# Optimization experiments

Hardware: AMD Instinct MI355X
Metric: run time of the kernel (lower is better)

Reference implementation:

```python
import jax, jax.numpy as jnp
import numpy as np

QMAX = 127.0
QMIN = -128.0


def setup_inputs() -> dict:
    key = jax.random.key(0)
    k1, k2, k3 = jax.random.split(key, 3)
    B, N, D, O = 4, 4096, 2048, 2048
    x = jax.random.normal(k1, (B, N, D), dtype=jnp.float32)
    weight = jax.random.normal(k2, (O, D), dtype=jnp.float32)
    bias = jax.random.normal(k3, (O,), dtype=jnp.float32)
    return {"x": x, "weight": weight, "bias": bias}


def reference(x, weight, bias):
    # --- per-row symmetric int8 quantization of the weight [O, D] ---
    w_max = jnp.clip(jnp.max(jnp.abs(weight), axis=1, keepdims=True), 1e-8, None)
    w_scale = (w_max / QMAX)                     # [O, 1]
    w_q = jnp.clip(jnp.round(weight / w_scale), QMIN, QMAX).astype(jnp.int8)
    w_scale = w_scale.squeeze(1).astype(jnp.float32)  # [O]

    # --- dynamic per-row symmetric int8 quantization of x [B, N, D] ---
    x_max = jnp.max(jnp.abs(x), axis=2, keepdims=True)       # [B, N, 1]
    x_scale = jnp.maximum(x_max / QMAX, 1e-12)               # [B, N, 1]
    x_q = jnp.clip(jnp.round(x / x_scale), QMIN, QMAX).astype(jnp.int8)

    # --- int8 GEMM accumulated in int32: [B,N,D] x [O,D]^T -> [B,N,O] ---
    acc = jnp.einsum("bnd,od->bno", x_q.astype(jnp.int32), w_q.astype(jnp.int32))

    # --- dequantize with per-row activation scale and per-out-channel weight scale ---
    y = acc.astype(jnp.float32) * x_scale.astype(jnp.float32) * w_scale[None, None, :]
    y = y + bias
    return y.astype(x.dtype)
```

## Files before the change

kernel.cpp:

```cpp
#include <hip/hip_runtime.h>
#include <stdint.h>
#include <stddef.h>

typedef int v4i __attribute__((ext_vector_type(4)));

#define GLOAD_LDS16(g, l) __builtin_amdgcn_global_load_lds( \
    (const __attribute__((address_space(1))) void*)(g),     \
    (__attribute__((address_space(3))) void*)(l), 16, 0, 0)

__device__ __forceinline__ int pack4(float4 f, float s) {
    int a = (int)rintf(f.x / s); a = a < -128 ? -128 : (a > 127 ? 127 : a);
    int b = (int)rintf(f.y / s); b = b < -128 ? -128 : (b > 127 ? 127 : b);
    int c = (int)rintf(f.z / s); c = c < -128 ? -128 : (c > 127 ? 127 : c);
    int d = (int)rintf(f.w / s); d = d < -128 ? -128 : (d > 127 ? 127 : d);
    return (a & 255) | ((b & 255) << 8) | ((c & 255) << 16) | ((d & 255) << 24);
}

__global__ __launch_bounds__(256) void quant_rows_2048(
    const float* __restrict__ in, signed char* __restrict__ q,
    float* __restrict__ scales, float floorv)
{
    const int lane = threadIdx.x & 63;
    const int row  = blockIdx.x * 4 + (threadIdx.x >> 6);
    const float* rp = in + (size_t)row * 2048;

    float4 v[8];
#pragma unroll
    for (int j = 0; j < 2; ++j) {
        const float4* p = (const float4*)(rp + j * 1024 + lane * 16);
#pragma unroll
        for (int i = 0; i < 4; ++i) v[j * 4 + i] = p[i];
    }
    float am = 0.0f;
#pragma unroll
    for (int i = 0; i < 8; ++i) {
        am = fmaxf(am, fabsf(v[i].x));
        am = fmaxf(am, fabsf(v[i].y));
        am = fmaxf(am, fabsf(v[i].z));
        am = fmaxf(am, fabsf(v[i].w));
    }
#pragma unroll
    for (int off = 32; off; off >>= 1) am = fmaxf(am, __shfl_xor(am, off));
    const float s = fmaxf(am / 127.0f, floorv);

#pragma unroll
    for (int j = 0; j < 2; ++j) {
        int4 pk;
        pk.x = pack4(v[j * 4 + 0], s);
        pk.y = pack4(v[j * 4 + 1], s);
        pk.z = pack4(v[j * 4 + 2], s);
        pk.w = pack4(v[j * 4 + 3], s);
        *(int4*)(q + (size_t)row * 2048 + j * 1024 + lane * 16) = pk;
    }
    if (lane == 0) scales[row] = s;
}

__global__ __launch_bounds__(512, 4) void gemm_i8_ring(
    const signed char* __restrict__ xq, const signed char* __restrict__ wq,
    const float* __restrict__ xs, const float* __restrict__ ws,
    const float* __restrict__ bias, float* __restrict__ out, int K)
{
    __shared__ __align__(16) signed char lds[73728];

    const int tid  = threadIdx.x;
    const int lane = tid & 63;
    const int wid  = tid >> 6;
    const int wm   = wid >> 2;
    const int wn   = wid & 3;

    const int nwg  = gridDim.x * gridDim.y;
    int orig = blockIdx.y * gridDim.x + blockIdx.x;
    int swz  = ((nwg & 7) == 0) ? ((orig & 7) * (nwg >> 3) + (orig >> 3)) : orig;
    const int brow = (swz / gridDim.x) * 128;
    const int bcol = (swz % gridDim.x) * 256;

    const int gch  = (((tid & 3) ^ ((tid >> 3) & 3)) << 4);
    const int lofs = tid << 4;
    const signed char* gA  = xq + (size_t)(brow + (tid >> 2)) * K;
    const signed char* gB0 = wq + (size_t)(bcol + (tid >> 2)) * K;
    const signed char* gB1 = wq + (size_t)(bcol + 128 + (tid >> 2)) * K;

#define BUFOFF(bb) ((bb) * 24576)
#define ST3(tt, bb) do {                                                         \
    GLOAD_LDS16(gA  + (size_t)(tt) * 64 + gch, lds + BUFOFF(bb) + lofs);         \
    GLOAD_LDS16(gB0 + (size_t)(tt) * 64 + gch, lds + BUFOFF(bb) + 8192 + lofs);  \
    GLOAD_LDS16(gB1 + (size_t)(tt) * 64 + gch, lds + BUFOFF(bb) + 16384 + lofs); \
} while (0)

    const int rl   = lane & 15;
    const int ko   = lane >> 4;
    const int slot = ((ko ^ ((rl >> 1) & 3)) << 4);

#define FRAG_A(bb, r) (*(const v4i*)(lds + BUFOFF(bb) + (r) * 64 + slot))
#define FRAG_B(bb, r) (*(const v4i*)(lds + BUFOFF(bb) + 8192 + (r) * 64 + slot))

    v4i acc[4][4] = {};
    const int ar = wm * 64 + rl;
    const int br = wn * 64 + rl;

    ST3(0, 0);
    ST3(1, 1);
    asm volatile("s_waitcnt vmcnt(3)" ::: "memory");
    __builtin_amdgcn_s_barrier();

    const int NT = K >> 6;
    for (int t = 0; t < NT; ++t) {
        const int buf = t % 3;

        v4i af[4], bf[4];
#pragma unroll
        for (int m = 0; m < 4; ++m) af[m] = FRAG_A(buf, ar + m * 16);
#pragma unroll
        for (int n = 0; n < 4; ++n) bf[n] = FRAG_B(buf, br + n * 16);

        if (t + 2 < NT) ST3(t + 2, (t + 2) % 3);

#pragma unroll
        for (int m = 0; m < 4; ++m)
#pragma unroll
            for (int n = 0; n < 4; ++n)
                acc[m][n] = __builtin_amdgcn_mfma_i32_16x16x64_i8(
                    af[m], bf[n], acc[m][n], 0, 0, 0);

        if (t + 2 < NT) {
            asm volatile("s_waitcnt vmcnt(3) lgkmcnt(0)" ::: "memory");
            __builtin_amdgcn_s_barrier();
        } else if (t + 2 == NT) {
            asm volatile("s_waitcnt vmcnt(0) lgkmcnt(0)" ::: "memory");
            __builtin_amdgcn_s_barrier();
        }
    }

    const int rg = lane >> 4;
#pragma unroll
    for (int n = 0; n < 4; ++n) {
        const int col = bcol + wn * 64 + n * 16 + rl;
        const float wsc = ws[col];
        const float bv  = bias[col];
#pragma unroll
        for (int m = 0; m < 4; ++m) {
#pragma unroll
            for (int j = 0; j < 4; ++j) {
                const int row = brow + wm * 64 + m * 16 + rg * 4 + j;
                out[(size_t)row * 2048 + col] =
                    (float)acc[m][n][j] * xs[row] * wsc + bv;
            }
        }
    }
#undef ST3
#undef BUFOFF
#undef FRAG_A
#undef FRAG_B
}

extern "C" void kernel_launch(void* const* d_in, const int* in_sizes, int n_in,
                              void* d_out, int out_size, void* d_ws, size_t ws_size,
                              hipStream_t stream) {
    const float* x    = (const float*)d_in[0];
    const float* w    = (const float*)d_in[1];
    const float* bias = (const float*)d_in[2];
    float* out = (float*)d_out;

    const int D = 2048;
    const int O = in_sizes[2];
    const int M = in_sizes[0] / D;

    char* wsb = (char*)d_ws;
    signed char* xq  = (signed char*)wsb;
    signed char* wqp = (signed char*)(wsb + (size_t)M * D);
    float* xs  = (float*)(wsb + (size_t)M * D + (size_t)O * D);
    float* wsc = (float*)(wsb + (size_t)M * D + (size_t)O * D + (size_t)M * 4);

    quant_rows_2048<<<M / 4, 256, 0, stream>>>(x, xq, xs, 1e-12f);
    quant_rows_2048<<<O / 4, 256, 0, stream>>>(w, wqp, wsc, 1e-8f / 127.0f);

    dim3 grid(O / 256, M / 128);
    gemm_i8_ring<<<grid, 512, 0, stream>>>(xq, wqp, xs, wsc, bias, out, D);
}
```

Before: 126.3 us.

## Shrink GEMM tile to 128x128 with 4 waves and fuse quant launches

The GEMM workgroup tile drops from 128x256 with 8 waves to 128x128 with 4 waves. Each wave still computes a 64x64 sub-tile, and the three-stage LDS ring shrinks to 48KB. The intent is to fit more workgroups per CU and spread the work over a grid twice as large, at the cost of less reuse of the A tile per block. The two quantization launches are also merged into a single kernel that picks x or w by block index, saving one launch.

```diff
diff --git a/kernel.cpp b/kernel.cpp
--- a/kernel.cpp
+++ b/kernel.cpp
@@ -16,12 +16,20 @@
     return (a & 255) | ((b & 255) << 8) | ((c & 255) << 16) | ((d & 255) << 24);
 }
 
-__global__ __launch_bounds__(256) void quant_rows_2048(
-    const float* __restrict__ in, signed char* __restrict__ q,
-    float* __restrict__ scales, float floorv)
+__global__ __launch_bounds__(256) void quant_both_2048(
+    const float* __restrict__ x, signed char* __restrict__ xq,
+    float* __restrict__ xs,
+    const float* __restrict__ w, signed char* __restrict__ wq,
+    float* __restrict__ wsc, int nx4)
 {
     const int lane = threadIdx.x & 63;
-    const int row  = blockIdx.x * 4 + (threadIdx.x >> 6);
+    const bool isx = ((int)blockIdx.x < nx4);
+    const int rb   = isx ? blockIdx.x : (blockIdx.x - nx4);
+    const int row  = rb * 4 + (threadIdx.x >> 6);
+    const float* in = isx ? x : w;
+    signed char* q  = isx ? xq : wq;
+    float* scales   = isx ? xs : wsc;
+    const float floorv = isx ? 1e-12f : (1e-8f / 127.0f);
     const float* rp = in + (size_t)row * 2048;
 
     float4 v[8];
@@ -55,52 +63,50 @@
     if (lane == 0) scales[row] = s;
 }
 
-__global__ __launch_bounds__(512, 4) void gemm_i8_ring(
+__global__ __launch_bounds__(256, 3) void gemm_i8_r3s(
     const signed char* __restrict__ xq, const signed char* __restrict__ wq,
     const float* __restrict__ xs, const float* __restrict__ ws,
     const float* __restrict__ bias, float* __restrict__ out, int K)
 {
-    __shared__ __align__(16) signed char lds[73728];
+    __shared__ __align__(16) signed char lds[49152];
 
     const int tid  = threadIdx.x;
     const int lane = tid & 63;
     const int wid  = tid >> 6;
-    const int wm   = wid >> 2;
-    const int wn   = wid & 3;
+    const int wm   = wid >> 1;
+    const int wn   = wid & 1;
 
     const int nwg  = gridDim.x * gridDim.y;
     int orig = blockIdx.y * gridDim.x + blockIdx.x;
     int swz  = ((nwg & 7) == 0) ? ((orig & 7) * (nwg >> 3) + (orig >> 3)) : orig;
     const int brow = (swz / gridDim.x) * 128;
-    const int bcol = (swz % gridDim.x) * 256;
+    const int bcol = (swz % gridDim.x) * 128;
 
-    const int gch  = (((tid & 3) ^ ((tid >> 3) & 3)) << 4);
-    const int lofs = tid << 4;
-    const signed char* gA  = xq + (size_t)(brow + (tid >> 2)) * K;
-    const signed char* gB0 = wq + (size_t)(bcol + (tid >> 2)) * K;
-    const signed char* gB1 = wq + (size_t)(bcol + 128 + (tid >> 2)) * K;
+    const int gch = (((tid & 3) ^ ((tid >> 3) & 3)) << 4);
+    const signed char* gA = xq + (size_t)(brow + (tid >> 2)) * K;
+    const signed char* gB = wq + (size_t)(bcol + (tid >> 2)) * K;
 
-#define BUFOFF(bb) ((bb) * 24576)
-#define ST3(tt, bb) do {                                                         \
-    GLOAD_LDS16(gA  + (size_t)(tt) * 64 + gch, lds + BUFOFF(bb) + lofs);         \
-    GLOAD_LDS16(gB0 + (size_t)(tt) * 64 + gch, lds + BUFOFF(bb) + 8192 + lofs);  \
-    GLOAD_LDS16(gB1 + (size_t)(tt) * 64 + gch, lds + BUFOFF(bb) + 16384 + lofs); \
+#define ST4(tt, bb) do {                                                                  \
+    GLOAD_LDS16(gA + (size_t)(tt) * 64 + gch,                  lds + (bb) * 16384 + (tid << 4));         \
+    GLOAD_LDS16(gA + (size_t)64 * K + (size_t)(tt) * 64 + gch, lds + (bb) * 16384 + 4096 + (tid << 4));  \
+    GLOAD_LDS16(gB + (size_t)(tt) * 64 + gch,                  lds + (bb) * 16384 + 8192 + (tid << 4));  \
+    GLOAD_LDS16(gB + (size_t)64 * K + (size_t)(tt) * 64 + gch, lds + (bb) * 16384 + 12288 + (tid << 4)); \
 } while (0)
 
     const int rl   = lane & 15;
     const int ko   = lane >> 4;
     const int slot = ((ko ^ ((rl >> 1) & 3)) << 4);
 
-#define FRAG_A(bb, r) (*(const v4i*)(lds + BUFOFF(bb) + (r) * 64 + slot))
-#define FRAG_B(bb, r) (*(const v4i*)(lds + BUFOFF(bb) + 8192 + (r) * 64 + slot))
+#define FRAG_A(bb, r) (*(const v4i*)(lds + (bb) * 16384 + (r) * 64 + slot))
+#define FRAG_B(bb, r) (*(const v4i*)(lds + (bb) * 16384 + 8192 + (r) * 64 + slot))
 
     v4i acc[4][4] = {};
     const int ar = wm * 64 + rl;
     const int br = wn * 64 + rl;
 
-    ST3(0, 0);
-    ST3(1, 1);
-    asm volatile("s_waitcnt vmcnt(3)" ::: "memory");
+    ST4(0, 0);
+    ST4(1, 1);
+    asm volatile("s_waitcnt vmcnt(4)" ::: "memory");
     __builtin_amdgcn_s_barrier();
 
     const int NT = K >> 6;
@@ -113,7 +119,7 @@
 #pragma unroll
         for (int n = 0; n < 4; ++n) bf[n] = FRAG_B(buf, br + n * 16);
 
-        if (t + 2 < NT) ST3(t + 2, (t + 2) % 3);
+        if (t + 2 < NT) ST4(t + 2, (t + 2) % 3);
 
 #pragma unroll
         for (int m = 0; m < 4; ++m)
@@ -123,7 +129,7 @@
                     af[m], bf[n], acc[m][n], 0, 0, 0);
 
         if (t + 2 < NT) {
-            asm volatile("s_waitcnt vmcnt(3) lgkmcnt(0)" ::: "memory");
+            asm volatile("s_waitcnt vmcnt(4) lgkmcnt(0)" ::: "memory");
             __builtin_amdgcn_s_barrier();
         } else if (t + 2 == NT) {
             asm volatile("s_waitcnt vmcnt(0) lgkmcnt(0)" ::: "memory");
@@ -147,8 +153,7 @@
             }
         }
     }
-#undef ST3
-#undef BUFOFF
+#undef ST4
 #undef FRAG_A
 #undef FRAG_B
 }
@@ -171,9 +176,8 @@
     float* xs  = (float*)(wsb + (size_t)M * D + (size_t)O * D);
     float* wsc = (float*)(wsb + (size_t)M * D + (size_t)O * D + (size_t)M * 4);
 
-    quant_rows_2048<<<M / 4, 256, 0, stream>>>(x, xq, xs, 1e-12f);
-    quant_rows_2048<<<O / 4, 256, 0, stream>>>(w, wqp, wsc, 1e-8f / 127.0f);
+    quant_both_2048<<<(M + O) / 4, 256, 0, stream>>>(x, xq, xs, w, wqp, wsc, M / 4);
 
-    dim3 grid(O / 256, M / 128);
-    gemm_i8_ring<<<grid, 512, 0, stream>>>(xq, wqp, xs, wsc, bias, out, D);
+    dim3 grid(O / 128, M / 128);
+    gemm_i8_r3s<<<grid, 256, 0, stream>>>(xq, wqp, xs, wsc, bias, out, D);
 }
```

Result: slower. 131.1 us (+3.8%).
